# Optimization experiments

Measured on AMD Instinct MI355X. Metric: run time of the kernel, lower is better.

## Reference

```python
import jax, jax.numpy as jnp
import numpy as np

NUM_EMB = 1024
EMB_DIM = 64


def setup_inputs() -> dict:
    key = jax.random.key(0)
    k1, k2 = jax.random.split(key)
    x = jax.random.normal(k1, (32, EMB_DIM, 4096), dtype=jnp.float32)
    # nn.Embedding weight initialized uniform(-1/K, 1/K)
    emb = jax.random.uniform(k2, (NUM_EMB, EMB_DIM), dtype=jnp.float32,
                             minval=-1.0 / NUM_EMB, maxval=1.0 / NUM_EMB)
    return {"x": x, "emb": emb}


def reference(x, emb):
    D = emb.shape[1]
    # Faithful to torch .view(-1, D): raw row-major flatten of contiguous x
    xf = x.reshape(-1, D)                                   # [N, D]
    # ||xf||^2 + ||e||^2 - 2 xf e^T  (cdist^2 via matmul)
    d = (jnp.sum(xf * xf, axis=1, keepdims=True)
         + jnp.sum(emb * emb, axis=1)
         - 2.0 * xf @ emb.T)                                # [N, K]
    idx = jnp.argmin(d, axis=1)                             # [N] int
    idx = idx.reshape((x.shape[0],) + x.shape[2:])          # [B, T]
    quantized = emb[idx].reshape(x.shape)                   # raw reshape, as view_as
    return quantized, idx
```

## Files before the change

### kernel.cpp

```cpp
#include <hip/hip_runtime.h>


#define N_ROWS   131072
#define NUM_EMB  1024
#define EMB_DIM  64
#define Q_ELEMS  8388608
#define THREADS  512
#define ROWS_PB  512
#define WCAP     3072

typedef short short8 __attribute__((ext_vector_type(8)));
typedef float f32x4  __attribute__((ext_vector_type(4)));

__device__ __forceinline__ unsigned short bf16_rne(float f) {
    unsigned u = __float_as_uint(f);
    u += 0x7fffu + ((u >> 16) & 1u);
    return (unsigned short)(u >> 16);
}

__device__ __forceinline__ unsigned fkey(float d) {
    unsigned b = __float_as_uint(d);
    return b ^ (((unsigned)((int)b >> 31)) | 0x80000000u);
}

__device__ __forceinline__ float np_sq64(const float* a) {
    #pragma clang fp contract(off)
    float r0=a[0]*a[0],r1=a[1]*a[1],r2=a[2]*a[2],r3=a[3]*a[3];
    float r4=a[4]*a[4],r5=a[5]*a[5],r6=a[6]*a[6],r7=a[7]*a[7];
    #pragma unroll
    for (int i=8;i<64;i+=8){
        r0+=a[i+0]*a[i+0];r1+=a[i+1]*a[i+1];r2+=a[i+2]*a[i+2];r3+=a[i+3]*a[i+3];
        r4+=a[i+4]*a[i+4];r5+=a[i+5]*a[i+5];r6+=a[i+6]*a[i+6];r7+=a[i+7]*a[i+7];
    }
    return ((r0+r1)+(r2+r3))+((r4+r5)+(r6+r7));
}

__device__ __forceinline__ float rotmin16(float v) {
    int x;
    x = __builtin_amdgcn_update_dpp(0, __float_as_int(v), 0x121, 0xf, 0xf, true);
    v = fminf(v, __int_as_float(x));
    x = __builtin_amdgcn_update_dpp(0, __float_as_int(v), 0x122, 0xf, 0xf, true);
    v = fminf(v, __int_as_float(x));
    x = __builtin_amdgcn_update_dpp(0, __float_as_int(v), 0x124, 0xf, 0xf, true);
    v = fminf(v, __int_as_float(x));
    x = __builtin_amdgcn_update_dpp(0, __float_as_int(v), 0x128, 0xf, 0xf, true);
    v = fminf(v, __int_as_float(x));
    return v;
}

__global__ __launch_bounds__(256) void vq_prep(const float* __restrict__ emb,
                                               float* __restrict__ sume,
                                               unsigned short* __restrict__ ehg) {
    int k = blockIdx.x * 256 + threadIdx.x;
    if (k < NUM_EMB) {
        sume[k] = np_sq64(emb + (k << 6));
        int c = k >> 7, krow = k & 127;
        #pragma unroll
        for (int gp = 0; gp < 8; ++gp) {
            short8 h;
            #pragma unroll
            for (int j = 0; j < 8; ++j)
                h[j] = (short)bf16_rne(emb[(k << 6) + gp*8 + j]);
            reinterpret_cast<short8*>(ehg)[c*1024 + gp*128 + krow] = h;
        }
    }
}

__global__ __launch_bounds__(THREADS, 2)
void vq_main(const float* __restrict__ x, const float* __restrict__ emb,
             const float* __restrict__ sume_g, const unsigned short* __restrict__ ehg,
             float* __restrict__ out_q, float* __restrict__ out_idx) {
    __shared__ int4     EH4[8192];
    __shared__ float    SUME[NUM_EMB];
    __shared__ float    RMIN[ROWS_PB];
    __shared__ float    SA[ROWS_PB];
    __shared__ int      WL[WCAP];
    __shared__ unsigned DMIN[ROWS_PB];
    __shared__ unsigned KMIN[ROWS_PB];
    __shared__ int      SIDX[ROWS_PB];
    __shared__ unsigned WCNT;

    const int t   = threadIdx.x;
    const int w   = t >> 6;
    const int l   = t & 63;
    const int g   = l >> 4;
    const int c16 = l & 15;
    const size_t blk_row0 = (size_t)blockIdx.x * ROWS_PB;

    const int4* eg4 = reinterpret_cast<const int4*>(ehg);
    #pragma unroll
    for (int i = 0; i < 16; ++i) EH4[t + i*THREADS] = eg4[t + i*THREADS];
    SUME[t]           = sume_g[t];
    SUME[t + THREADS] = sume_g[t + THREADS];
    DMIN[t] = 0xFFFFFFFFu; KMIN[t] = 0xFFFFFFFFu;
    if (t == 0) WCNT = 0u;

    short8 ah[4][2];
    #pragma unroll
    for (int st = 0; st < 4; ++st) {
        const float* xp = x + (blk_row0 + (size_t)(w*64 + st*16 + c16)) * EMB_DIM;
        float sabs = 0.f;
        #pragma unroll
        for (int hf = 0; hf < 2; ++hf) {
            #pragma unroll
            for (int j = 0; j < 8; ++j) {
                float v = 2.0f * xp[hf*32 + g*8 + j];
                sabs += fabsf(v);
                ah[st][hf][j] = (short)bf16_rne(v);
            }
        }
        sabs += __shfl_xor(sabs, 16);
        sabs += __shfl_xor(sabs, 32);
        if (g == 0) SA[w*64 + st*16 + c16] = sabs;
    }
    __syncthreads();

    float stash[4][4];
    #pragma unroll
    for (int st = 0; st < 4; ++st)
        #pragma unroll
        for (int r = 0; r < 4; ++r) stash[st][r] = 3.4e38f;

    const short8* EHs = reinterpret_cast<const short8*>(EH4);
    #pragma unroll 4
    for (int lt = 0; lt < 64; ++lt) {
        const int ub = (lt >> 3)*1024 + (lt & 7)*16 + c16;
        short8 bh0 = EHs[ub + (g    )*128];
        short8 bh1 = EHs[ub + (g + 4)*128];
        float scol = SUME[lt*16 + c16];
        #pragma unroll
        for (int st = 0; st < 4; ++st) {
            f32x4 a = {0.f,0.f,0.f,0.f};
            a = __builtin_amdgcn_mfma_f32_16x16x32_bf16(ah[st][0], bh0, a, 0,0,0);
            a = __builtin_amdgcn_mfma_f32_16x16x32_bf16(ah[st][1], bh1, a, 0,0,0);
            #pragma unroll
            for (int r = 0; r < 4; ++r)
                stash[st][r] = fminf(stash[st][r], scol - a[r]);
        }
    }

    #pragma unroll
    for (int st = 0; st < 4; ++st) {
        #pragma unroll
        for (int r = 0; r < 4; ++r) {
            float v = rotmin16(stash[st][r]);
            if (c16 == 0) RMIN[w*64 + st*16 + 4*g + r] = v;
        }
    }
    __syncthreads();
    RMIN[t] = RMIN[t] + (SA[t] * 1.6e-5f + 4.0e-5f);
    __syncthreads();

    float thrv[4][4], thrmax[4];
    #pragma unroll
    for (int st = 0; st < 4; ++st) {
        #pragma unroll
        for (int r = 0; r < 4; ++r) thrv[st][r] = RMIN[w*64 + st*16 + 4*g + r];
        thrmax[st] = fmaxf(fmaxf(thrv[st][0], thrv[st][1]),
                           fmaxf(thrv[st][2], thrv[st][3]));
    }

    #pragma unroll 2
    for (int lt = 0; lt < 64; ++lt) {
        const int ub = (lt >> 3)*1024 + (lt & 7)*16 + c16;
        short8 bh0 = EHs[ub + (g    )*128];
        short8 bh1 = EHs[ub + (g + 4)*128];
        float scol = SUME[lt*16 + c16];
        const int kk = lt*16 + c16;
        #pragma unroll
        for (int st = 0; st < 4; ++st) {
            f32x4 a = {0.f,0.f,0.f,0.f};
            a = __builtin_amdgcn_mfma_f32_16x16x32_bf16(ah[st][0], bh0, a, 0,0,0);
            a = __builtin_amdgcn_mfma_f32_16x16x32_bf16(ah[st][1], bh1, a, 0,0,0);
            float s0 = scol - a[0], s1 = scol - a[1];
            float s2 = scol - a[2], s3 = scol - a[3];
            float m4 = fminf(fminf(s0, s1), fminf(s2, s3));
            if (m4 < thrmax[st]) {
                const int rb = (w*64 + st*16 + 4*g) << 10;
                if (s0 < thrv[st][0]) { unsigned q = atomicAdd(&WCNT,1u); if (q<WCAP) WL[q] = rb + (0<<10) + kk; }
                if (s1 < thrv[st][1]) { unsigned q = atomicAdd(&WCNT,1u); if (q<WCAP) WL[q] = rb + (1<<10) + kk; }
                if (s2 < thrv[st][2]) { unsigned q = atomicAdd(&WCNT,1u); if (q<WCAP) WL[q] = rb + (2<<10) + kk; }
                if (s3 < thrv[st][3]) { unsigned q = atomicAdd(&WCNT,1u); if (q<WCAP) WL[q] = rb + (3<<10) + kk; }
            }
        }
    }
    __syncthreads();

    const unsigned wc = WCNT;
    float* WLD = reinterpret_cast<float*>(EH4);

    if (wc <= WCAP) {
        for (unsigned q = t; q < wc; q += THREADS) {
            int pr = WL[q]; int row = pr >> 10; int kk = pr & 1023;
            const float* xr = x + (blk_row0 + (size_t)row) * EMB_DIM;
            const float* er = emb + (kk << 6);
            float sumx = np_sq64(xr);
            float cc = 0.f;
            #pragma unroll 8
            for (int i = 0; i < EMB_DIM; ++i)
                cc = fmaf(2.0f * xr[i], er[i], cc);
            float d;
            {
                #pragma clang fp contract(off)
                d = (sumx + SUME[kk]) - cc;
            }
            WLD[q] = d;
            atomicMin(&DMIN[row], fkey(d));
        }
        __syncthreads();
        for (unsigned q = t; q < wc; q += THREADS) {
            int pr = WL[q]; int row = pr >> 10; int kk = pr & 1023;
            if (fkey(WLD[q]) == DMIN[row])
                atomicMin(&KMIN[row], (unsigned)kk);
        }
        __syncthreads();
        int bk = (int)KMIN[t];
        SIDX[t] = bk;
        out_idx[blk_row0 + t] = (float)bk;
    } else {
        const float* xr = x + (blk_row0 + (size_t)t) * EMB_DIM;
        float sumx = np_sq64(xr);
        volatile const float* xv = xr;
        float bm = 3.4e38f; int bb = 0;
        for (int kk = 0; kk < NUM_EMB; ++kk) {
            const float* er = emb + (kk << 6);
            float cc = 0.f;
            for (int i = 0; i < EMB_DIM; ++i)
                cc = fmaf(2.0f * xv[i], er[i], cc);
            {
                #pragma clang fp contract(off)
                float d = (sumx + SUME[kk]) - cc;
                if (d < bm) { bm = d; bb = kk; }
            }
        }
        SIDX[t] = bb;
        out_idx[blk_row0 + t] = (float)bb;
    }
    __syncthreads();

    const float4* emb4 = reinterpret_cast<const float4*>(emb);
    float4* q4 = reinterpret_cast<float4*>(out_q + blk_row0 * EMB_DIM);
    #pragma unroll
    for (int i = 0; i < 16; ++i) {
        int e4 = t + i * THREADS;
        int rr = e4 >> 4, cc2 = e4 & 15;
        q4[e4] = emb4[SIDX[rr]*16 + cc2];
    }
}

extern "C" void kernel_launch(void* const* d_in, const int* in_sizes, int n_in,
                              void* d_out, int out_size, void* d_ws, size_t ws_size,
                              hipStream_t stream) {
    const float* x   = (const float*)d_in[0];
    const float* emb = (const float*)d_in[1];
    float* out_q   = (float*)d_out;
    float* out_idx = out_q + Q_ELEMS;
    float*          sume = (float*)d_ws;
    unsigned short* ehg  = (unsigned short*)((char*)d_ws + 4096);

    vq_prep<<<dim3(NUM_EMB / 256), dim3(256), 0, stream>>>(emb, sume, ehg);
    vq_main<<<dim3(N_ROWS / ROWS_PB), dim3(THREADS), 0, stream>>>(x, emb, sume, ehg,
                                                                  out_q, out_idx);
}
```

Before: 101.9 us.

## Split codebook across two wave halves with 1024-thread blocks and vectorized x loads

Doubles the block to 1024 threads and gives each half of the waves half of the codebook columns for both MFMA passes. The two halves' partial row minima are merged through shared memory before the threshold is built. x rows are now loaded as float4 instead of scalar loads. The aim is to halve the per-wave MFMA loop length and add latency hiding. In exchange each wave redundantly loads and converts the same x rows, register pressure per thread rises under the 1024-thread bound, and the fallback path leaves half the threads idle.

Result: faster. 86.35 us (-15.3%).

```diff
diff --git a/kernel.cpp b/kernel.cpp
--- a/kernel.cpp
+++ b/kernel.cpp
@@ -5,7 +5,7 @@
 #define NUM_EMB  1024
 #define EMB_DIM  64
 #define Q_ELEMS  8388608
-#define THREADS  512
+#define THREADS  1024
 #define ROWS_PB  512
 #define WCAP     3072
 
@@ -66,13 +66,14 @@
     }
 }
 
-__global__ __launch_bounds__(THREADS, 2)
+__global__ __launch_bounds__(THREADS)
 void vq_main(const float* __restrict__ x, const float* __restrict__ emb,
              const float* __restrict__ sume_g, const unsigned short* __restrict__ ehg,
              float* __restrict__ out_q, float* __restrict__ out_idx) {
     __shared__ int4     EH4[8192];
     __shared__ float    SUME[NUM_EMB];
-    __shared__ float    RMIN[ROWS_PB];
+    __shared__ float    LM[2][ROWS_PB];
+    __shared__ float    THR[ROWS_PB];
     __shared__ float    SA[ROWS_PB];
     __shared__ int      WL[WCAP];
     __shared__ unsigned DMIN[ROWS_PB];
@@ -80,38 +81,43 @@
     __shared__ int      SIDX[ROWS_PB];
     __shared__ unsigned WCNT;
 
-    const int t   = threadIdx.x;
-    const int w   = t >> 6;
-    const int l   = t & 63;
-    const int g   = l >> 4;
-    const int c16 = l & 15;
+    const int t    = threadIdx.x;
+    const int w    = t >> 6;
+    const int w8   = w & 7;
+    const int half = w >> 3;
+    const int l    = t & 63;
+    const int g    = l >> 4;
+    const int c16  = l & 15;
     const size_t blk_row0 = (size_t)blockIdx.x * ROWS_PB;
 
     const int4* eg4 = reinterpret_cast<const int4*>(ehg);
     #pragma unroll
-    for (int i = 0; i < 16; ++i) EH4[t + i*THREADS] = eg4[t + i*THREADS];
-    SUME[t]           = sume_g[t];
-    SUME[t + THREADS] = sume_g[t + THREADS];
-    DMIN[t] = 0xFFFFFFFFu; KMIN[t] = 0xFFFFFFFFu;
+    for (int i = 0; i < 8; ++i) EH4[t + i*THREADS] = eg4[t + i*THREADS];
+    SUME[t] = sume_g[t];
+    if (t < ROWS_PB) { DMIN[t] = 0xFFFFFFFFu; KMIN[t] = 0xFFFFFFFFu; }
     if (t == 0) WCNT = 0u;
 
     short8 ah[4][2];
     #pragma unroll
     for (int st = 0; st < 4; ++st) {
-        const float* xp = x + (blk_row0 + (size_t)(w*64 + st*16 + c16)) * EMB_DIM;
+        const float4* xq = reinterpret_cast<const float4*>(
+            x + (blk_row0 + (size_t)(w8*64 + st*16 + c16)) * EMB_DIM);
         float sabs = 0.f;
         #pragma unroll
         for (int hf = 0; hf < 2; ++hf) {
+            float4 u0 = xq[hf*8 + g*2 + 0];
+            float4 u1 = xq[hf*8 + g*2 + 1];
+            float vv[8] = {u0.x,u0.y,u0.z,u0.w,u1.x,u1.y,u1.z,u1.w};
             #pragma unroll
             for (int j = 0; j < 8; ++j) {
-                float v = 2.0f * xp[hf*32 + g*8 + j];
+                float v = 2.0f * vv[j];
                 sabs += fabsf(v);
                 ah[st][hf][j] = (short)bf16_rne(v);
             }
         }
         sabs += __shfl_xor(sabs, 16);
         sabs += __shfl_xor(sabs, 32);
-        if (g == 0) SA[w*64 + st*16 + c16] = sabs;
+        if (g == 0 && half == 0) SA[w8*64 + st*16 + c16] = sabs;
     }
     __syncthreads();
 
@@ -123,11 +129,12 @@
 
     const short8* EHs = reinterpret_cast<const short8*>(EH4);
     #pragma unroll 4
-    for (int lt = 0; lt < 64; ++lt) {
-        const int ub = (lt >> 3)*1024 + (lt & 7)*16 + c16;
+    for (int lt = 0; lt < 32; ++lt) {
+        const int ltg = half*32 + lt;
+        const int ub  = (ltg >> 3)*1024 + (ltg & 7)*16 + c16;
         short8 bh0 = EHs[ub + (g    )*128];
         short8 bh1 = EHs[ub + (g + 4)*128];
-        float scol = SUME[lt*16 + c16];
+        float scol = SUME[ltg*16 + c16];
         #pragma unroll
         for (int st = 0; st < 4; ++st) {
             f32x4 a = {0.f,0.f,0.f,0.f};
@@ -144,29 +151,33 @@
         #pragma unroll
         for (int r = 0; r < 4; ++r) {
             float v = rotmin16(stash[st][r]);
-            if (c16 == 0) RMIN[w*64 + st*16 + 4*g + r] = v;
-        }
-    }
-    __syncthreads();
-    RMIN[t] = RMIN[t] + (SA[t] * 1.6e-5f + 4.0e-5f);
+            if (c16 == 0) LM[half][w8*64 + st*16 + 4*g + r] = v;
+        }
+    }
+    __syncthreads();
+    if (t < ROWS_PB) {
+        float bm = fminf(LM[0][t], LM[1][t]);
+        THR[t] = bm + (SA[t] * 1.6e-5f + 4.0e-5f);
+    }
     __syncthreads();
 
     float thrv[4][4], thrmax[4];
     #pragma unroll
     for (int st = 0; st < 4; ++st) {
         #pragma unroll
-        for (int r = 0; r < 4; ++r) thrv[st][r] = RMIN[w*64 + st*16 + 4*g + r];
+        for (int r = 0; r < 4; ++r) thrv[st][r] = THR[w8*64 + st*16 + 4*g + r];
         thrmax[st] = fmaxf(fmaxf(thrv[st][0], thrv[st][1]),
                            fmaxf(thrv[st][2], thrv[st][3]));
     }
 
     #pragma unroll 2
-    for (int lt = 0; lt < 64; ++lt) {
-        const int ub = (lt >> 3)*1024 + (lt & 7)*16 + c16;
+    for (int lt = 0; lt < 32; ++lt) {
+        const int ltg = half*32 + lt;
+        const int ub  = (ltg >> 3)*1024 + (ltg & 7)*16 + c16;
         short8 bh0 = EHs[ub + (g    )*128];
         short8 bh1 = EHs[ub + (g + 4)*128];
-        float scol = SUME[lt*16 + c16];
-        const int kk = lt*16 + c16;
+        float scol = SUME[ltg*16 + c16];
+        const int kk = ltg*16 + c16;
         #pragma unroll
         for (int st = 0; st < 4; ++st) {
             f32x4 a = {0.f,0.f,0.f,0.f};
@@ -176,7 +187,7 @@
             float s2 = scol - a[2], s3 = scol - a[3];
             float m4 = fminf(fminf(s0, s1), fminf(s2, s3));
             if (m4 < thrmax[st]) {
-                const int rb = (w*64 + st*16 + 4*g) << 10;
+                const int rb = (w8*64 + st*16 + 4*g) << 10;
                 if (s0 < thrv[st][0]) { unsigned q = atomicAdd(&WCNT,1u); if (q<WCAP) WL[q] = rb + (0<<10) + kk; }
                 if (s1 < thrv[st][1]) { unsigned q = atomicAdd(&WCNT,1u); if (q<WCAP) WL[q] = rb + (1<<10) + kk; }
                 if (s2 < thrv[st][2]) { unsigned q = atomicAdd(&WCNT,1u); if (q<WCAP) WL[q] = rb + (2<<10) + kk; }
@@ -214,34 +225,38 @@
                 atomicMin(&KMIN[row], (unsigned)kk);
         }
         __syncthreads();
-        int bk = (int)KMIN[t];
-        SIDX[t] = bk;
-        out_idx[blk_row0 + t] = (float)bk;
+        if (t < ROWS_PB) {
+            int bk = (int)KMIN[t];
+            SIDX[t] = bk;
+            out_idx[blk_row0 + t] = (float)bk;
+        }
     } else {
-        const float* xr = x + (blk_row0 + (size_t)t) * EMB_DIM;
-        float sumx = np_sq64(xr);
-        volatile const float* xv = xr;
-        float bm = 3.4e38f; int bb = 0;
-        for (int kk = 0; kk < NUM_EMB; ++kk) {
-            const float* er = emb + (kk << 6);
-            float cc = 0.f;
-            for (int i = 0; i < EMB_DIM; ++i)
-                cc = fmaf(2.0f * xv[i], er[i], cc);
-            {
-                #pragma clang fp contract(off)
-                float d = (sumx + SUME[kk]) - cc;
-                if (d < bm) { bm = d; bb = kk; }
-            }
-        }
-        SIDX[t] = bb;
-        out_idx[blk_row0 + t] = (float)bb;
+        if (t < ROWS_PB) {
+            const float* xr = x + (blk_row0 + (size_t)t) * EMB_DIM;
+            float sumx = np_sq64(xr);
+            volatile const float* xv = xr;
+            float bm = 3.4e38f; int bb = 0;
+            for (int kk = 0; kk < NUM_EMB; ++kk) {
+                const float* er = emb + (kk << 6);
+                float cc = 0.f;
+                for (int i = 0; i < EMB_DIM; ++i)
+                    cc = fmaf(2.0f * xv[i], er[i], cc);
+                {
+                    #pragma clang fp contract(off)
+                    float d = (sumx + SUME[kk]) - cc;
+                    if (d < bm) { bm = d; bb = kk; }
+                }
+            }
+            SIDX[t] = bb;
+            out_idx[blk_row0 + t] = (float)bb;
+        }
     }
     __syncthreads();
 
     const float4* emb4 = reinterpret_cast<const float4*>(emb);
     float4* q4 = reinterpret_cast<float4*>(out_q + blk_row0 * EMB_DIM);
     #pragma unroll
-    for (int i = 0; i < 16; ++i) {
+    for (int i = 0; i < 8; ++i) {
         int e4 = t + i * THREADS;
         int rr = e4 >> 4, cc2 = e4 & 15;
         q4[e4] = emb4[SIDX[rr]*16 + cc2];
```
